# Kernel tuning notes

Measured on AMD Instinct MI355X. Metric: run time of the kernel, lower is better.

Reference implementation:

```python
import jax, jax.numpy as jnp
import numpy as np

N_NODES = 50000
N_EDGES = 800000
N_FEAT = 128
HIDDEN = 16
N_CLASSES = 16


def spline_conv(x, src, dst, u, weight, root, bias, num_nodes):
    """SplineConv, dim=1, kernel_size=2, degree=1, open spline, aggr='mean'.

    x: [N, in], weight: [2, in, out], u: [E, 1] pseudo-coords in [0, 1).
    Linear B-spline basis over 2 knots: basis = (1-u, u) -> W[0], W[1].
    Transform at node level first (cheaper than per-edge when E > N),
    then gather along edges and scatter-mean to targets.
    """
    h = jnp.einsum('ni,kio->kno', x, weight)  # [2, N, out]
    msg = (1.0 - u) * h[0][src] + u * h[1][src]  # [E, out]
    agg = jax.ops.segment_sum(msg, dst, num_segments=num_nodes)
    deg = jax.ops.segment_sum(jnp.ones((src.shape[0],), x.dtype), dst,
                              num_segments=num_nodes)
    agg = agg / jnp.maximum(deg, 1.0)[:, None]
    return agg + x @ root + bias


def setup_inputs() -> dict:
    key = jax.random.key(0)
    ks = jax.random.split(key, 8)
    x = jax.random.normal(ks[0], (N_NODES, N_FEAT), dtype=jnp.float32)
    edge_index = jax.random.randint(ks[1], (2, N_EDGES), 0, N_NODES, dtype=jnp.int32)
    edge_attr = jax.random.uniform(ks[2], (N_EDGES, 1), dtype=jnp.float32)
    s1 = 1.0 / np.sqrt(N_FEAT)
    s2 = 1.0 / np.sqrt(HIDDEN)
    return {
        'x': x,
        'edge_index': edge_index,
        'edge_attr': edge_attr,
        'w1': jax.random.normal(ks[3], (2, N_FEAT, HIDDEN), dtype=jnp.float32) * s1,
        'root1': jax.random.normal(ks[4], (N_FEAT, HIDDEN), dtype=jnp.float32) * s1,
        'b1': jnp.zeros((HIDDEN,), dtype=jnp.float32),
        'w2': jax.random.normal(ks[5], (2, HIDDEN, N_CLASSES), dtype=jnp.float32) * s2,
        'root2': jax.random.normal(ks[6], (HIDDEN, N_CLASSES), dtype=jnp.float32) * s2,
        'b2': jnp.zeros((N_CLASSES,), dtype=jnp.float32),
    }


def reference(x, edge_index, edge_attr, w1, root1, b1, w2, root2, b2):
    src, dst = edge_index[0], edge_index[1]
    n = x.shape[0]
    # eval mode: F.dropout(training=False) is identity
    h = jax.nn.elu(spline_conv(x, src, dst, edge_attr, w1, root1, b1, n))
    out = spline_conv(h, src, dst, edge_attr, w2, root2, b2, n)
    return jax.nn.log_softmax(out, axis=1)
```

## Files before the change

kernel.cpp:

```cpp
#include <hip/hip_runtime.h>
#include <hip/hip_bf16.h>
#include <math.h>

#define N_NODES 50000
#define N_EDGES 800000
#define N_FEAT 128
#define HIDDEN 16
#define N_CLASSES 16

#define NBUCK 782
#define PB_NB 196
#define PB_E  4096
#define BCAP  1600

typedef __attribute__((ext_vector_type(8))) short short8v;
typedef __attribute__((ext_vector_type(4))) float floatx4;

__device__ __forceinline__ float bf2f(unsigned int bits16) {
    return __uint_as_float(bits16 << 16);
}
__device__ __forceinline__ unsigned int f2bf_bits(float f) {
    __hip_bfloat16 h = __float2bfloat16(f);
    return (unsigned int)*reinterpret_cast<unsigned short*>(&h);
}

__global__ __launch_bounds__(256) void k_node1(
    const float* __restrict__ x, const float* __restrict__ w1,
    const float* __restrict__ root1, const float* __restrict__ b1,
    unsigned int* __restrict__ ABu, float* __restrict__ C)
{
    int lane = threadIdx.x & 63;
    int wid  = threadIdx.x >> 6;
    int m = lane & 15;
    int q = lane >> 4;
    int nb = blockIdx.x * 64 + wid * 16;

    short8v bf[3][4];
#pragma unroll
    for (int c = 0; c < 4; ++c) {
        int k0 = c * 32 + q * 8;
        const float* p0 = w1 + (size_t)k0 * 16 + m;
        const float* p1 = w1 + 2048 + (size_t)k0 * 16 + m;
        const float* p2 = root1 + (size_t)k0 * 16 + m;
#pragma unroll
        for (int j = 0; j < 8; ++j) {
            bf[0][c][j] = (short)f2bf_bits(p0[j * 16]);
            bf[1][c][j] = (short)f2bf_bits(p1[j * 16]);
            bf[2][c][j] = (short)f2bf_bits(p2[j * 16]);
        }
    }

    int row = min(nb + m, N_NODES - 1);
    const float* xr = x + (size_t)row * N_FEAT;
    short8v af[4];
#pragma unroll
    for (int c = 0; c < 4; ++c) {
        int k0 = c * 32 + q * 8;
        float4 v0 = *(const float4*)(xr + k0);
        float4 v1 = *(const float4*)(xr + k0 + 4);
        af[c][0] = (short)f2bf_bits(v0.x); af[c][1] = (short)f2bf_bits(v0.y);
        af[c][2] = (short)f2bf_bits(v0.z); af[c][3] = (short)f2bf_bits(v0.w);
        af[c][4] = (short)f2bf_bits(v1.x); af[c][5] = (short)f2bf_bits(v1.y);
        af[c][6] = (short)f2bf_bits(v1.z); af[c][7] = (short)f2bf_bits(v1.w);
    }

    floatx4 acc0 = {0.f, 0.f, 0.f, 0.f};
    floatx4 acc1 = {0.f, 0.f, 0.f, 0.f};
    floatx4 acc2 = {0.f, 0.f, 0.f, 0.f};
#pragma unroll
    for (int c = 0; c < 4; ++c) {
        acc0 = __builtin_amdgcn_mfma_f32_16x16x32_bf16(af[c], bf[0][c], acc0, 0, 0, 0);
        acc1 = __builtin_amdgcn_mfma_f32_16x16x32_bf16(af[c], bf[1][c], acc1, 0, 0, 0);
        acc2 = __builtin_amdgcn_mfma_f32_16x16x32_bf16(af[c], bf[2][c], acc2, 0, 0, 0);
    }

    float bo = b1[m];
#pragma unroll
    for (int j = 0; j < 4; ++j) {
        int n = nb + q * 4 + j;
        if (n < N_NODES) {
            ABu[(size_t)n * 16 + m] = (f2bf_bits(acc1[j]) << 16) | f2bf_bits(acc0[j]);
            C[(size_t)n * 16 + m]   = acc2[j] + bo;
        }
    }
}

__global__ __launch_bounds__(256) void k_part(
    const int* __restrict__ src, const int* __restrict__ dst,
    const float* __restrict__ u, int* __restrict__ rank,
    int2* __restrict__ epb)
{
    __shared__ int cnt[NBUCK];
    for (int i = threadIdx.x; i < NBUCK; i += 256) cnt[i] = 0;
    __syncthreads();
    int ebase = blockIdx.x * PB_E;
    int myd[PB_E / 256];
#pragma unroll
    for (int k = 0; k < PB_E / 256; ++k) {
        int e = ebase + k * 256 + threadIdx.x;
        myd[k] = (e < N_EDGES) ? dst[e] : -1;
        if (myd[k] >= 0) atomicAdd(&cnt[myd[k] >> 6], 1);
    }
    __syncthreads();
    for (int i = threadIdx.x; i < NBUCK; i += 256) {
        int c = cnt[i];
        int base = (c > 0) ? atomicAdd(&rank[i], c) : 0;
        cnt[i] = i * BCAP + base;
    }
    __syncthreads();
#pragma unroll
    for (int k = 0; k < PB_E / 256; ++k) {
        if (myd[k] >= 0) {
            int e = ebase + k * 256 + threadIdx.x;
            int b = myd[k] >> 6;
            int pos = atomicAdd(&cnt[b], 1);
            if (pos < (b + 1) * BCAP)
                epb[pos] = make_int2((src[e] & 0xFFFF) | ((myd[k] & 63) << 16),
                                     __float_as_int(u[e]));
        }
    }
}

__global__ __launch_bounds__(256) void k_bsort(
    const int* __restrict__ rank, int2* __restrict__ epb,
    int* __restrict__ rowbeg, int* __restrict__ rowend)
{
    __shared__ int2 buf[BCAP];
    __shared__ int2 sorted[BCAP];
    __shared__ int cnt[64], cur[64];
    int b = blockIdx.x;
    int beg = b * BCAP;
    int m = min(rank[b], BCAP);

    if (threadIdx.x < 64) cnt[threadIdx.x] = 0;
    __syncthreads();
    for (int i = threadIdx.x; i < m; i += 256) {
        int2 p = epb[beg + i];
        buf[i] = p;
        atomicAdd(&cnt[(p.x >> 16) & 63], 1);
    }
    __syncthreads();
    if (threadIdx.x < 64) {
        int v = cnt[threadIdx.x];
        int s = v;
#pragma unroll
        for (int off = 1; off < 64; off <<= 1) {
            int w = __shfl_up(s, off);
            if (threadIdx.x >= off) s += w;
        }
        int ex = s - v;
        cur[threadIdx.x] = ex;
        int n = (b << 6) + threadIdx.x;
        if (n < N_NODES) {
            rowbeg[n] = beg + ex;
            rowend[n] = beg + ex + v;
        }
    }
    __syncthreads();
    for (int i = threadIdx.x; i < m; i += 256) {
        int2 p = buf[i];
        int pos = atomicAdd(&cur[(p.x >> 16) & 63], 1);
        sorted[pos] = p;
    }
    __syncthreads();
    for (int i = threadIdx.x; i < m; i += 256)
        epb[beg + i] = sorted[i];
}

__global__ __launch_bounds__(256) void k_gfused1(
    const int* __restrict__ rowbeg, const int* __restrict__ rowend,
    const int2* __restrict__ ep, const unsigned int* __restrict__ ABu,
    const float* __restrict__ C, const float* __restrict__ w2,
    const float* __restrict__ root2, const float* __restrict__ b2,
    unsigned int* __restrict__ ABu2, float* __restrict__ C2)
{
    __shared__ float W2s[16 * 48];
    for (int t = threadIdx.x; t < 16 * 48; t += 256) {
        int j = t / 48, o = t % 48;
        float v;
        if (o < 16)       v = w2[j * 16 + o];
        else if (o < 32)  v = w2[256 + j * 16 + (o - 16)];
        else              v = root2[j * 16 + (o - 32)];
        W2s[t] = v;
    }
    __syncthreads();

    int n    = (blockIdx.x * 256 + threadIdx.x) >> 6;
    int lane = threadIdx.x & 63;
    int g = lane >> 3;
    int l = lane & 7;
    int beg = rowbeg[n], end = rowend[n];
    const uint2* AB2 = (const uint2*)ABu;
    float ax = 0.f, ay = 0.f;
    int e = beg + g;
    for (; e + 8 < end; e += 16) {
        int2 p0 = ep[e];
        int2 p1 = ep[e + 8];
        float u0 = __int_as_float(p0.y);
        float u1 = __int_as_float(p1.y);
        uint2 q0 = AB2[(size_t)(p0.x & 0xFFFF) * 8 + l];
        uint2 q1 = AB2[(size_t)(p1.x & 0xFFFF) * 8 + l];
        ax += (1.f - u0) * bf2f(q0.x & 0xFFFF) + u0 * bf2f(q0.x >> 16);
        ay += (1.f - u0) * bf2f(q0.y & 0xFFFF) + u0 * bf2f(q0.y >> 16);
        ax += (1.f - u1) * bf2f(q1.x & 0xFFFF) + u1 * bf2f(q1.x >> 16);
        ay += (1.f - u1) * bf2f(q1.y & 0xFFFF) + u1 * bf2f(q1.y >> 16);
    }
    if (e < end) {
        int2 p0 = ep[e];
        float u0 = __int_as_float(p0.y);
        uint2 q0 = AB2[(size_t)(p0.x & 0xFFFF) * 8 + l];
        ax += (1.f - u0) * bf2f(q0.x & 0xFFFF) + u0 * bf2f(q0.x >> 16);
        ay += (1.f - u0) * bf2f(q0.y & 0xFFFF) + u0 * bf2f(q0.y >> 16);
    }
#pragma unroll
    for (int s = 8; s < 64; s <<= 1) {
        ax += __shfl_xor(ax, s);
        ay += __shfl_xor(ay, s);
    }
    float dv = fmaxf((float)(end - beg), 1.f);
    float2 cv = *(const float2*)&C[(size_t)n * 16 + 2 * l];
    float pre0 = ax / dv + cv.x;
    float pre1 = ay / dv + cv.y;
    float h0 = pre0 > 0.f ? pre0 : expm1f(pre0);
    float h1 = pre1 > 0.f ? pre1 : expm1f(pre1);

    int oc = (lane < 48) ? lane : 0;
    float val = 0.f;
#pragma unroll
    for (int j2 = 0; j2 < 8; ++j2) {
        float hh0 = __shfl(h0, j2);
        float hh1 = __shfl(h1, j2);
        val += hh0 * W2s[(2 * j2) * 48 + oc] + hh1 * W2s[(2 * j2 + 1) * 48 + oc];
    }
    float bval = __shfl(val, (lane + 16) & 63);
    if (lane < 16)
        ABu2[(size_t)n * 16 + lane] = (f2bf_bits(bval) << 16) | f2bf_bits(val);
    else if (lane >= 32 && lane < 48)
        C2[(size_t)n * 16 + (lane - 32)] = val + b2[lane - 32];
}

__global__ __launch_bounds__(256) void k_gather2(
    const int* __restrict__ rowbeg, const int* __restrict__ rowend,
    const int2* __restrict__ ep, const unsigned int* __restrict__ ABu,
    const float* __restrict__ C, float* __restrict__ out)
{
    int n    = (blockIdx.x * 256 + threadIdx.x) >> 6;
    int lane = threadIdx.x & 63;
    int g = lane >> 3;
    int l = lane & 7;
    int beg = rowbeg[n], end = rowend[n];
    const uint2* AB2 = (const uint2*)ABu;
    float ax = 0.f, ay = 0.f;
    int e = beg + g;
    for (; e + 8 < end; e += 16) {
        int2 p0 = ep[e];
        int2 p1 = ep[e + 8];
        float u0 = __int_as_float(p0.y);
        float u1 = __int_as_float(p1.y);
        uint2 q0 = AB2[(size_t)(p0.x & 0xFFFF) * 8 + l];
        uint2 q1 = AB2[(size_t)(p1.x & 0xFFFF) * 8 + l];
        ax += (1.f - u0) * bf2f(q0.x & 0xFFFF) + u0 * bf2f(q0.x >> 16);
        ay += (1.f - u0) * bf2f(q0.y & 0xFFFF) + u0 * bf2f(q0.y >> 16);
        ax += (1.f - u1) * bf2f(q1.x & 0xFFFF) + u1 * bf2f(q1.x >> 16);
        ay += (1.f - u1) * bf2f(q1.y & 0xFFFF) + u1 * bf2f(q1.y >> 16);
    }
    if (e < end) {
        int2 p0 = ep[e];
        float u0 = __int_as_float(p0.y);
        uint2 q0 = AB2[(size_t)(p0.x & 0xFFFF) * 8 + l];
        ax += (1.f - u0) * bf2f(q0.x & 0xFFFF) + u0 * bf2f(q0.x >> 16);
        ay += (1.f - u0) * bf2f(q0.y & 0xFFFF) + u0 * bf2f(q0.y >> 16);
    }
#pragma unroll
    for (int s = 8; s < 64; s <<= 1) {
        ax += __shfl_xor(ax, s);
        ay += __shfl_xor(ay, s);
    }
    float dv = fmaxf((float)(end - beg), 1.f);
    float2 cv = *(const float2*)&C[(size_t)n * 16 + 2 * l];
    float v0 = ax / dv + cv.x;
    float v1 = ay / dv + cv.y;

    float m = fmaxf(v0, v1);
#pragma unroll
    for (int s = 1; s < 8; s <<= 1) m = fmaxf(m, __shfl_xor(m, s));
    float ssum = __expf(v0 - m) + __expf(v1 - m);
#pragma unroll
    for (int s = 1; s < 8; s <<= 1) ssum += __shfl_xor(ssum, s);
    float lse = m + __logf(ssum);
    if (lane < 8)
        *(float2*)&out[(size_t)n * 16 + 2 * l] = make_float2(v0 - lse, v1 - lse);
}

extern "C" void kernel_launch(void* const* d_in, const int* in_sizes, int n_in,
                              void* d_out, int out_size, void* d_ws, size_t ws_size,
                              hipStream_t stream) {
    const float* x     = (const float*)d_in[0];
    const int*   ei    = (const int*)d_in[1];
    const float* ea    = (const float*)d_in[2];
    const float* w1    = (const float*)d_in[3];
    const float* root1 = (const float*)d_in[4];
    const float* b1    = (const float*)d_in[5];
    const float* w2    = (const float*)d_in[6];
    const float* root2 = (const float*)d_in[7];
    const float* b2    = (const float*)d_in[8];
    float* out = (float*)d_out;

    char* ws = (char*)d_ws;
    unsigned int* ABu  = (unsigned int*)ws;
    unsigned int* ABu2 = ABu + (size_t)N_NODES * 16;
    float* C    = (float*)(ABu2 + (size_t)N_NODES * 16);
    float* C2   = C + (size_t)N_NODES * 16;
    int2*  EPB  = (int2*)(C2 + (size_t)N_NODES * 16);
    int* RANK   = (int*)(EPB + (size_t)NBUCK * BCAP);
    int* ROWBEG = RANK + NBUCK;
    int* ROWEND = ROWBEG + N_NODES;

    const int* srcp = ei;
    const int* dstp = ei + N_EDGES;

    hipMemsetAsync(RANK, 0, NBUCK * sizeof(int), stream);

    k_node1<<<782, 256, 0, stream>>>(x, w1, root1, b1, ABu, C);
    k_part<<<PB_NB, 256, 0, stream>>>(srcp, dstp, ea, RANK, EPB);
    k_bsort<<<NBUCK, 256, 0, stream>>>(RANK, EPB, ROWBEG, ROWEND);
    k_gfused1<<<N_NODES / 4, 256, 0, stream>>>(ROWBEG, ROWEND, EPB, ABu, C,
                                               w2, root2, b2, ABu2, C2);
    k_gather2<<<N_NODES / 4, 256, 0, stream>>>(ROWBEG, ROWEND, EPB, ABu2, C2, out);
}
```

Baseline: 96.46 us.

## Compress edge records to 32 bits and stage layer-1 weights in LDS

The bucket sort now writes a separate 4-byte edge array that packs the 16-bit source index with the pseudo-coordinate quantized to 16 bits. It also packs row begin and degree into one word per node. Both gather kernels read these compact records, which halves edge-stream traffic and drops one index load per node. The node transform kernel loads and converts the weights once per block into padded shared memory instead of every lane doing strided global loads into registers. Quantizing u to 16 bits adds a small approximation error.

```diff
diff --git a/kernel.cpp b/kernel.cpp
--- a/kernel.cpp
+++ b/kernel.cpp
@@ -29,26 +29,23 @@
     const float* __restrict__ root1, const float* __restrict__ b1,
     unsigned int* __restrict__ ABu, float* __restrict__ C)
 {
+    __shared__ unsigned short Wl[48 * 136];
+    for (int t = threadIdx.x; t < 48 * 128; t += 256) {
+        int o = t >> 7;
+        int i = t & 127;
+        float v;
+        if (o < 16)       v = w1[i * 16 + o];
+        else if (o < 32)  v = w1[2048 + i * 16 + (o - 16)];
+        else              v = root1[i * 16 + (o - 32)];
+        Wl[o * 136 + i] = (unsigned short)f2bf_bits(v);
+    }
+    __syncthreads();
+
     int lane = threadIdx.x & 63;
     int wid  = threadIdx.x >> 6;
     int m = lane & 15;
     int q = lane >> 4;
     int nb = blockIdx.x * 64 + wid * 16;
-
-    short8v bf[3][4];
-#pragma unroll
-    for (int c = 0; c < 4; ++c) {
-        int k0 = c * 32 + q * 8;
-        const float* p0 = w1 + (size_t)k0 * 16 + m;
-        const float* p1 = w1 + 2048 + (size_t)k0 * 16 + m;
-        const float* p2 = root1 + (size_t)k0 * 16 + m;
-#pragma unroll
-        for (int j = 0; j < 8; ++j) {
-            bf[0][c][j] = (short)f2bf_bits(p0[j * 16]);
-            bf[1][c][j] = (short)f2bf_bits(p1[j * 16]);
-            bf[2][c][j] = (short)f2bf_bits(p2[j * 16]);
-        }
-    }
 
     int row = min(nb + m, N_NODES - 1);
     const float* xr = x + (size_t)row * N_FEAT;
@@ -69,9 +66,13 @@
     floatx4 acc2 = {0.f, 0.f, 0.f, 0.f};
 #pragma unroll
     for (int c = 0; c < 4; ++c) {
-        acc0 = __builtin_amdgcn_mfma_f32_16x16x32_bf16(af[c], bf[0][c], acc0, 0, 0, 0);
-        acc1 = __builtin_amdgcn_mfma_f32_16x16x32_bf16(af[c], bf[1][c], acc1, 0, 0, 0);
-        acc2 = __builtin_amdgcn_mfma_f32_16x16x32_bf16(af[c], bf[2][c], acc2, 0, 0, 0);
+        int ko = c * 32 + q * 8;
+        short8v b0 = *(const short8v*)&Wl[(0 * 16 + m) * 136 + ko];
+        short8v b1f = *(const short8v*)&Wl[(1 * 16 + m) * 136 + ko];
+        short8v b2f = *(const short8v*)&Wl[(2 * 16 + m) * 136 + ko];
+        acc0 = __builtin_amdgcn_mfma_f32_16x16x32_bf16(af[c], b0, acc0, 0, 0, 0);
+        acc1 = __builtin_amdgcn_mfma_f32_16x16x32_bf16(af[c], b1f, acc1, 0, 0, 0);
+        acc2 = __builtin_amdgcn_mfma_f32_16x16x32_bf16(af[c], b2f, acc2, 0, 0, 0);
     }
 
     float bo = b1[m];
@@ -122,11 +123,11 @@
 }
 
 __global__ __launch_bounds__(256) void k_bsort(
-    const int* __restrict__ rank, int2* __restrict__ epb,
-    int* __restrict__ rowbeg, int* __restrict__ rowend)
+    const int* __restrict__ rank, const int2* __restrict__ epb,
+    unsigned int* __restrict__ epc, unsigned int* __restrict__ rowpack)
 {
     __shared__ int2 buf[BCAP];
-    __shared__ int2 sorted[BCAP];
+    __shared__ unsigned int sortc[BCAP];
     __shared__ int cnt[64], cur[64];
     int b = blockIdx.x;
     int beg = b * BCAP;
@@ -151,27 +152,27 @@
         int ex = s - v;
         cur[threadIdx.x] = ex;
         int n = (b << 6) + threadIdx.x;
-        if (n < N_NODES) {
-            rowbeg[n] = beg + ex;
-            rowend[n] = beg + ex + v;
-        }
+        if (n < N_NODES)
+            rowpack[n] = (unsigned int)(beg + ex) | ((unsigned int)v << 21);
     }
     __syncthreads();
     for (int i = threadIdx.x; i < m; i += 256) {
         int2 p = buf[i];
         int pos = atomicAdd(&cur[(p.x >> 16) & 63], 1);
-        sorted[pos] = p;
+        float uv = __int_as_float(p.y);
+        unsigned int u16 = (unsigned int)(uv * 65535.f + 0.5f);
+        sortc[pos] = ((unsigned int)p.x & 0xFFFFu) | (u16 << 16);
     }
     __syncthreads();
     for (int i = threadIdx.x; i < m; i += 256)
-        epb[beg + i] = sorted[i];
+        epc[beg + i] = sortc[i];
 }
 
 __global__ __launch_bounds__(256) void k_gfused1(
-    const int* __restrict__ rowbeg, const int* __restrict__ rowend,
-    const int2* __restrict__ ep, const unsigned int* __restrict__ ABu,
-    const float* __restrict__ C, const float* __restrict__ w2,
-    const float* __restrict__ root2, const float* __restrict__ b2,
+    const unsigned int* __restrict__ rowpack, const unsigned int* __restrict__ ep,
+    const unsigned int* __restrict__ ABu, const float* __restrict__ C,
+    const float* __restrict__ w2, const float* __restrict__ root2,
+    const float* __restrict__ b2,
     unsigned int* __restrict__ ABu2, float* __restrict__ C2)
 {
     __shared__ float W2s[16 * 48];
@@ -189,26 +190,30 @@
     int lane = threadIdx.x & 63;
     int g = lane >> 3;
     int l = lane & 7;
-    int beg = rowbeg[n], end = rowend[n];
+    unsigned int rp = rowpack[n];
+    int beg = (int)(rp & 0x1FFFFFu);
+    int deg = (int)(rp >> 21);
+    int end = beg + deg;
     const uint2* AB2 = (const uint2*)ABu;
+    const float uscale = 1.f / 65535.f;
     float ax = 0.f, ay = 0.f;
     int e = beg + g;
     for (; e + 8 < end; e += 16) {
-        int2 p0 = ep[e];
-        int2 p1 = ep[e + 8];
-        float u0 = __int_as_float(p0.y);
-        float u1 = __int_as_float(p1.y);
-        uint2 q0 = AB2[(size_t)(p0.x & 0xFFFF) * 8 + l];
-        uint2 q1 = AB2[(size_t)(p1.x & 0xFFFF) * 8 + l];
+        unsigned int p0 = ep[e];
+        unsigned int p1 = ep[e + 8];
+        float u0 = (float)(p0 >> 16) * uscale;
+        float u1 = (float)(p1 >> 16) * uscale;
+        uint2 q0 = AB2[(size_t)(p0 & 0xFFFF) * 8 + l];
+        uint2 q1 = AB2[(size_t)(p1 & 0xFFFF) * 8 + l];
         ax += (1.f - u0) * bf2f(q0.x & 0xFFFF) + u0 * bf2f(q0.x >> 16);
         ay += (1.f - u0) * bf2f(q0.y & 0xFFFF) + u0 * bf2f(q0.y >> 16);
         ax += (1.f - u1) * bf2f(q1.x & 0xFFFF) + u1 * bf2f(q1.x >> 16);
         ay += (1.f - u1) * bf2f(q1.y & 0xFFFF) + u1 * bf2f(q1.y >> 16);
     }
     if (e < end) {
-        int2 p0 = ep[e];
-        float u0 = __int_as_float(p0.y);
-        uint2 q0 = AB2[(size_t)(p0.x & 0xFFFF) * 8 + l];
+        unsigned int p0 = ep[e];
+        float u0 = (float)(p0 >> 16) * uscale;
+        uint2 q0 = AB2[(size_t)(p0 & 0xFFFF) * 8 + l];
         ax += (1.f - u0) * bf2f(q0.x & 0xFFFF) + u0 * bf2f(q0.x >> 16);
         ay += (1.f - u0) * bf2f(q0.y & 0xFFFF) + u0 * bf2f(q0.y >> 16);
     }
@@ -217,7 +222,7 @@
         ax += __shfl_xor(ax, s);
         ay += __shfl_xor(ay, s);
     }
-    float dv = fmaxf((float)(end - beg), 1.f);
+    float dv = fmaxf((float)deg, 1.f);
     float2 cv = *(const float2*)&C[(size_t)n * 16 + 2 * l];
     float pre0 = ax / dv + cv.x;
     float pre1 = ay / dv + cv.y;
@@ -240,34 +245,38 @@
 }
 
 __global__ __launch_bounds__(256) void k_gather2(
-    const int* __restrict__ rowbeg, const int* __restrict__ rowend,
-    const int2* __restrict__ ep, const unsigned int* __restrict__ ABu,
-    const float* __restrict__ C, float* __restrict__ out)
+    const unsigned int* __restrict__ rowpack, const unsigned int* __restrict__ ep,
+    const unsigned int* __restrict__ ABu, const float* __restrict__ C,
+    float* __restrict__ out)
 {
     int n    = (blockIdx.x * 256 + threadIdx.x) >> 6;
     int lane = threadIdx.x & 63;
     int g = lane >> 3;
     int l = lane & 7;
-    int beg = rowbeg[n], end = rowend[n];
+    unsigned int rp = rowpack[n];
+    int beg = (int)(rp & 0x1FFFFFu);
+    int deg = (int)(rp >> 21);
+    int end = beg + deg;
     const uint2* AB2 = (const uint2*)ABu;
+    const float uscale = 1.f / 65535.f;
     float ax = 0.f, ay = 0.f;
     int e = beg + g;
     for (; e + 8 < end; e += 16) {
-        int2 p0 = ep[e];
-        int2 p1 = ep[e + 8];
-        float u0 = __int_as_float(p0.y);
-        float u1 = __int_as_float(p1.y);
-        uint2 q0 = AB2[(size_t)(p0.x & 0xFFFF) * 8 + l];
-        uint2 q1 = AB2[(size_t)(p1.x & 0xFFFF) * 8 + l];
+        unsigned int p0 = ep[e];
+        unsigned int p1 = ep[e + 8];
+        float u0 = (float)(p0 >> 16) * uscale;
+        float u1 = (float)(p1 >> 16) * uscale;
+        uint2 q0 = AB2[(size_t)(p0 & 0xFFFF) * 8 + l];
+        uint2 q1 = AB2[(size_t)(p1 & 0xFFFF) * 8 + l];
         ax += (1.f - u0) * bf2f(q0.x & 0xFFFF) + u0 * bf2f(q0.x >> 16);
         ay += (1.f - u0) * bf2f(q0.y & 0xFFFF) + u0 * bf2f(q0.y >> 16);
         ax += (1.f - u1) * bf2f(q1.x & 0xFFFF) + u1 * bf2f(q1.x >> 16);
         ay += (1.f - u1) * bf2f(q1.y & 0xFFFF) + u1 * bf2f(q1.y >> 16);
     }
     if (e < end) {
-        int2 p0 = ep[e];
-        float u0 = __int_as_float(p0.y);
-        uint2 q0 = AB2[(size_t)(p0.x & 0xFFFF) * 8 + l];
+        unsigned int p0 = ep[e];
+        float u0 = (float)(p0 >> 16) * uscale;
+        uint2 q0 = AB2[(size_t)(p0 & 0xFFFF) * 8 + l];
         ax += (1.f - u0) * bf2f(q0.x & 0xFFFF) + u0 * bf2f(q0.x >> 16);
         ay += (1.f - u0) * bf2f(q0.y & 0xFFFF) + u0 * bf2f(q0.y >> 16);
     }
@@ -276,7 +285,7 @@
         ax += __shfl_xor(ax, s);
         ay += __shfl_xor(ay, s);
     }
-    float dv = fmaxf((float)(end - beg), 1.f);
+    float dv = fmaxf((float)deg, 1.f);
     float2 cv = *(const float2*)&C[(size_t)n * 16 + 2 * l];
     float v0 = ax / dv + cv.x;
     float v1 = ay / dv + cv.y;
@@ -312,9 +321,9 @@
     float* C    = (float*)(ABu2 + (size_t)N_NODES * 16);
     float* C2   = C + (size_t)N_NODES * 16;
     int2*  EPB  = (int2*)(C2 + (size_t)N_NODES * 16);
-    int* RANK   = (int*)(EPB + (size_t)NBUCK * BCAP);
-    int* ROWBEG = RANK + NBUCK;
-    int* ROWEND = ROWBEG + N_NODES;
+    unsigned int* EPC = (unsigned int*)(EPB + (size_t)NBUCK * BCAP);
+    int* RANK   = (int*)(EPC + (size_t)NBUCK * BCAP);
+    unsigned int* ROWPACK = (unsigned int*)(RANK + NBUCK);
 
     const int* srcp = ei;
     const int* dstp = ei + N_EDGES;
@@ -323,8 +332,8 @@
 
     k_node1<<<782, 256, 0, stream>>>(x, w1, root1, b1, ABu, C);
     k_part<<<PB_NB, 256, 0, stream>>>(srcp, dstp, ea, RANK, EPB);
-    k_bsort<<<NBUCK, 256, 0, stream>>>(RANK, EPB, ROWBEG, ROWEND);
-    k_gfused1<<<N_NODES / 4, 256, 0, stream>>>(ROWBEG, ROWEND, EPB, ABu, C,
+    k_bsort<<<NBUCK, 256, 0, stream>>>(RANK, EPB, EPC, ROWPACK);
+    k_gfused1<<<N_NODES / 4, 256, 0, stream>>>(ROWPACK, EPC, ABu, C,
                                                w2, root2, b2, ABu2, C2);
-    k_gather2<<<N_NODES / 4, 256, 0, stream>>>(ROWBEG, ROWEND, EPB, ABu2, C2, out);
-}
+    k_gather2<<<N_NODES / 4, 256, 0, stream>>>(ROWPACK, EPC, ABu2, C2, out);
+}
```

Result: slower. 102.9 us (+6.7%).
